# Optimization experiments

Measured on AMD Instinct MI355X. Metric: run time of the kernel, lower is better.

Reference implementation:

```python
import jax, jax.numpy as jnp
import numpy as np

N_NODES = 100000
N_EDGES = 1600000
IN_CH = 128
EDGE_CH = 32
HEADS = 4
OUT_CH = 32
NEG_SLOPE = 0.2
EPS = 1e-16  # matches torch_geometric softmax denominator epsilon


def setup_inputs() -> dict:
    key = jax.random.key(0)
    ks = jax.random.split(key, 8)
    x = jax.random.normal(ks[0], (N_NODES, IN_CH), dtype=jnp.float32)
    edge_attr = jax.random.normal(ks[1], (N_EDGES, EDGE_CH), dtype=jnp.float32)
    # glorot-ish scaled params
    Wl = jax.random.normal(ks[2], (HEADS * OUT_CH, IN_CH), dtype=jnp.float32) * (1.0 / np.sqrt(IN_CH))
    We = jax.random.normal(ks[3], (HEADS * OUT_CH, EDGE_CH), dtype=jnp.float32) * (1.0 / np.sqrt(EDGE_CH))
    att_l = jax.random.normal(ks[4], (1, HEADS, OUT_CH), dtype=jnp.float32) * 0.1
    att_r = jax.random.normal(ks[5], (1, HEADS, OUT_CH), dtype=jnp.float32) * 0.1
    att_e = jax.random.normal(ks[6], (1, HEADS, OUT_CH), dtype=jnp.float32) * 0.1
    bias = jnp.zeros((HEADS * OUT_CH,), dtype=jnp.float32)
    edge_index = jax.random.randint(ks[7], (2, N_EDGES), 0, N_NODES, dtype=jnp.int32)
    return {"x": x, "edge_attr": edge_attr, "Wl": Wl, "We": We,
            "att_l": att_l, "att_r": att_r, "att_e": att_e,
            "bias": bias, "edge_index": edge_index}


def reference(x, edge_attr, Wl, We, att_l, att_r, att_e, bias, edge_index):
    N = x.shape[0]
    H, C = att_l.shape[1], att_l.shape[2]
    # shared lin_l == lin_r projection  [N, H, C]
    xl = (x @ Wl.T).reshape(N, H, C)
    alpha_l = (xl * att_l).sum(-1)          # [N, H] source term
    alpha_r = (xl * att_r).sum(-1)          # [N, H] target term
    # edge feature projection            [E, H, C]
    e = (edge_attr @ We.T).reshape(-1, H, C)
    alpha_e = (e * att_e).sum(-1)           # [E, H]
    src, dst = edge_index[0], edge_index[1]
    # per-edge attention logits
    alpha = alpha_l[src] + alpha_r[dst] + alpha_e        # [E, H]
    alpha = jax.nn.leaky_relu(alpha, NEG_SLOPE)
    # segment softmax over incoming edges of each target node
    amax = jax.ops.segment_max(alpha, dst, num_segments=N)   # [N, H]
    ex = jnp.exp(alpha - amax[dst])
    denom = jax.ops.segment_sum(ex, dst, num_segments=N)     # [N, H]
    alpha_n = ex / (denom[dst] + EPS)                        # [E, H]
    # weighted scatter-add aggregation of source features
    msg = xl[src] * alpha_n[:, :, None]                      # [E, H, C]
    out = jax.ops.segment_sum(msg, dst, num_segments=N)      # [N, H, C]
    out = out.reshape(N, H * C) + bias                       # concat heads
    return out
```

## Files before the change

### kernel.cpp

```cpp
#include <hip/hip_runtime.h>
#include <hip/hip_fp16.h>

#define NN 100000
#define NE 1600000
#define NB 391
#define NEG 0.2f
#define NHALF 50000

#define OFF_XLB   ((size_t)0)
#define OFF_AL    ((size_t)6400000)
#define OFF_AR    ((size_t)6800000)
#define OFF_WE    ((size_t)7200000)
#define OFF_RECP  ((size_t)7200128)
#define OFF_RECS  ((size_t)10400128)
#define OFF_PAL   ((size_t)12000128)
#define OFF_TMP   OFF_RECP
#define OFF_BSUM  (OFF_RECP + 110000)
#define OFF_DEG   ((size_t)15200128)
#define OFF_ROW   ((size_t)15300128)

__device__ __forceinline__ unsigned short f2bf(float f) {
    unsigned u = __float_as_uint(f);
    u += 0x7fffu + ((u >> 16) & 1u);
    return (unsigned short)(u >> 16);
}
__device__ __forceinline__ float bf2f(unsigned short v) {
    return __uint_as_float((unsigned)v << 16);
}

__global__ void k_prep_zero(const float* __restrict__ We, const float* __restrict__ att_e,
                            float* __restrict__ we, int* __restrict__ deg) {
    int i = blockIdx.x * 256 + threadIdx.x;
    if (i < NN) deg[i] = 0;
    if (blockIdx.x == 0 && threadIdx.x < 128) {
        int t = threadIdx.x, h = t >> 5, k = t & 31;
        float s = 0.f;
        for (int c = 0; c < 32; ++c)
            s += att_e[h * 32 + c] * We[(size_t)(h * 32 + c) * 32 + k];
        we[t] = s;
    }
}

__global__ __launch_bounds__(256, 2) void k_node(
        const float* __restrict__ x, const float* __restrict__ Wl,
        const float* __restrict__ attl, const float* __restrict__ attr_,
        unsigned short* __restrict__ xlb, float* __restrict__ al, float* __restrict__ ar) {
    __shared__ float wT[128 * 128];
    __shared__ float xT[128 * 32];
    int t = threadIdx.x;
    int og = t & 31, ng = t >> 5;
    int nb = blockIdx.x * 32;

    {
        int o = t & 127, q = t >> 7;
        #pragma unroll
        for (int chunk = 0; chunk < 16; ++chunk) {
            int k0 = chunk * 8 + q * 4;
            float4 w = *(const float4*)&Wl[(size_t)o * 128 + k0];
            wT[(k0 + 0) * 128 + o] = w.x;
            wT[(k0 + 1) * 128 + o] = w.y;
            wT[(k0 + 2) * 128 + o] = w.z;
            wT[(k0 + 3) * 128 + o] = w.w;
        }
    }
    {
        int n = t & 31, q = t >> 5;
        #pragma unroll
        for (int chunk = 0; chunk < 4; ++chunk) {
            int k0 = chunk * 32 + q * 4;
            float4 v = *(const float4*)&x[(size_t)(nb + n) * 128 + k0];
            xT[(k0 + 0) * 32 + n] = v.x;
            xT[(k0 + 1) * 32 + n] = v.y;
            xT[(k0 + 2) * 32 + n] = v.z;
            xT[(k0 + 3) * 32 + n] = v.w;
        }
    }
    float4 attl4 = *(const float4*)&attl[og * 4];
    float4 attr4 = *(const float4*)&attr_[og * 4];
    __syncthreads();

    float4 a0 = make_float4(0,0,0,0), a1 = a0, a2 = a0, a3 = a0;
    #pragma unroll 8
    for (int k = 0; k < 128; ++k) {
        float4 w  = *(const float4*)&wT[k * 128 + og * 4];
        float4 xv = *(const float4*)&xT[k * 32  + ng * 4];
        a0.x += w.x * xv.x; a0.y += w.y * xv.x; a0.z += w.z * xv.x; a0.w += w.w * xv.x;
        a1.x += w.x * xv.y; a1.y += w.y * xv.y; a1.z += w.z * xv.y; a1.w += w.w * xv.y;
        a2.x += w.x * xv.z; a2.y += w.y * xv.z; a2.z += w.z * xv.z; a2.w += w.w * xv.z;
        a3.x += w.x * xv.w; a3.y += w.y * xv.w; a3.z += w.z * xv.w; a3.w += w.w * xv.w;
    }

    float4 accs[4] = {a0, a1, a2, a3};
    #pragma unroll
    for (int j = 0; j < 4; ++j) {
        int node = nb + ng * 4 + j;
        ushort4 pk;
        pk.x = f2bf(accs[j].x); pk.y = f2bf(accs[j].y);
        pk.z = f2bf(accs[j].z); pk.w = f2bf(accs[j].w);
        *(ushort4*)&xlb[(size_t)node * 128 + og * 4] = pk;
        float pl = accs[j].x * attl4.x + accs[j].y * attl4.y +
                   accs[j].z * attl4.z + accs[j].w * attl4.w;
        float pr = accs[j].x * attr4.x + accs[j].y * attr4.y +
                   accs[j].z * attr4.z + accs[j].w * attr4.w;
        #pragma unroll
        for (int off = 1; off <= 4; off <<= 1) {
            pl += __shfl_xor(pl, off);
            pr += __shfl_xor(pr, off);
        }
        if ((og & 7) == 0) {
            al[(size_t)node * 4 + (og >> 3)] = pl;
            ar[(size_t)node * 4 + (og >> 3)] = pr;
        }
    }
}

__global__ __launch_bounds__(256) void k_alpha(
        const float* __restrict__ eattr, const int* __restrict__ ei,
        const float* __restrict__ al, const float* __restrict__ ar,
        const float* __restrict__ we, int* __restrict__ deg,
        float2* __restrict__ palpha) {
    __shared__ __align__(16) float wsh[128];
    if (threadIdx.x < 128) wsh[threadIdx.x] = we[threadIdx.x];
    __syncthreads();
    int e = blockIdx.x * 256 + threadIdx.x;
    int src = ei[e], dst = ei[NE + e];
    const float4* ea = (const float4*)(eattr + (size_t)e * 32);
    float a[4] = {0.f, 0.f, 0.f, 0.f};
    #pragma unroll
    for (int r = 0; r < 8; ++r) {
        float4 v = ea[r];
        #pragma unroll
        for (int h = 0; h < 4; ++h) {
            float4 w = *(const float4*)&wsh[h * 32 + r * 4];
            a[h] += v.x * w.x + v.y * w.y + v.z * w.z + v.w * w.w;
        }
    }
    float4 ls = *(const float4*)&al[(size_t)src * 4];
    float4 rs = *(const float4*)&ar[(size_t)dst * 4];
    a[0] += ls.x + rs.x; a[1] += ls.y + rs.y;
    a[2] += ls.z + rs.z; a[3] += ls.w + rs.w;
    #pragma unroll
    for (int h = 0; h < 4; ++h) {
        float v = a[h] > 0.f ? a[h] : NEG * a[h];
        a[h] = __expf(fminf(v, 60.f));
    }
    __half2 h01 = __floats2half2_rn(a[0], a[1]);
    __half2 h23 = __floats2half2_rn(a[2], a[3]);
    float2 p;
    p.x = *reinterpret_cast<float*>(&h01);
    p.y = *reinterpret_cast<float*>(&h23);
    palpha[e] = p;
    atomicAdd(&deg[dst], 1);
}

__global__ void k_scan_block(const int* __restrict__ deg, int* __restrict__ row_tmp,
                             int* __restrict__ bsum) {
    __shared__ int sh[256];
    int t = threadIdx.x, i = blockIdx.x * 256 + t;
    int d = (i < NN) ? deg[i] : 0;
    int v = d;
    sh[t] = v; __syncthreads();
    for (int off = 1; off < 256; off <<= 1) {
        int add = (t >= off) ? sh[t - off] : 0;
        __syncthreads();
        v += add; sh[t] = v; __syncthreads();
    }
    if (i < NN) row_tmp[i] = v - d;
    if (t == 255) bsum[blockIdx.x] = v;
}

__global__ void k_scan_top(int* __restrict__ bsum) {
    __shared__ int sh[512];
    int t = threadIdx.x;
    int d = (t < NB) ? bsum[t] : 0;
    int v = d;
    sh[t] = v; __syncthreads();
    for (int off = 1; off < 512; off <<= 1) {
        int add = (t >= off) ? sh[t - off] : 0;
        __syncthreads();
        v += add; sh[t] = v; __syncthreads();
    }
    if (t < NB) bsum[t] = v - d;
}

__global__ void k_scan_add(const int* __restrict__ row_tmp, const int* __restrict__ bsum,
                           int* __restrict__ row, int* __restrict__ cursor) {
    int i = blockIdx.x * 256 + threadIdx.x;
    if (i < NN) {
        int v = row_tmp[i] + bsum[i >> 8];
        row[i] = v;
        cursor[i] = v;
    }
    if (i == 0) row[NN] = NE;
}

__global__ __launch_bounds__(256) void k_scat(
        const int* __restrict__ ei, const float2* __restrict__ palpha,
        int* __restrict__ cursor, int* __restrict__ rec_src,
        float2* __restrict__ rec_p, int lo, int hi) {
    int e = blockIdx.x * 256 + threadIdx.x;
    int dst = ei[NE + e];
    int src = ei[e];
    float2 p = palpha[e];
    if (dst >= lo && dst < hi) {
        int slot = atomicAdd(&cursor[dst], 1);
        rec_src[slot] = src;
        rec_p[slot] = p;
    }
}

__device__ __forceinline__ float pick_p(float2 q, int h) {
    __half2 h01 = *reinterpret_cast<const __half2*>(&q.x);
    __half2 h23 = *reinterpret_cast<const __half2*>(&q.y);
    float2 p01 = __half22float2(h01);
    float2 p23 = __half22float2(h23);
    float lo = (h & 2) ? p23.x : p01.x;
    float hi = (h & 2) ? p23.y : p01.y;
    return (h & 1) ? hi : lo;
}

__global__ __launch_bounds__(128) void k_out(
        const int* __restrict__ row, const int* __restrict__ rec_src,
        const float2* __restrict__ rec_p, const unsigned short* __restrict__ xlb,
        const float* __restrict__ bias, float* __restrict__ out) {
    int n = blockIdx.x;
    int t = threadIdx.x, h = t >> 5;
    int s0 = row[n], s1 = row[n + 1];

    float l0 = 0.f, l1 = 0.f, l2 = 0.f, l3 = 0.f;
    float O0 = 0.f, O1 = 0.f, O2 = 0.f, O3 = 0.f;
    int s = s0;
    for (; s + 4 <= s1; s += 4) {
        int src0 = rec_src[s + 0], src1 = rec_src[s + 1];
        int src2 = rec_src[s + 2], src3 = rec_src[s + 3];
        float2 q0 = rec_p[s + 0], q1 = rec_p[s + 1];
        float2 q2 = rec_p[s + 2], q3 = rec_p[s + 3];
        unsigned short v0 = xlb[(size_t)src0 * 128 + t];
        unsigned short v1 = xlb[(size_t)src1 * 128 + t];
        unsigned short v2 = xlb[(size_t)src2 * 128 + t];
        unsigned short v3 = xlb[(size_t)src3 * 128 + t];
        float p0 = pick_p(q0, h), p1 = pick_p(q1, h);
        float p2 = pick_p(q2, h), p3 = pick_p(q3, h);
        l0 += p0; l1 += p1; l2 += p2; l3 += p3;
        O0 += p0 * bf2f(v0); O1 += p1 * bf2f(v1);
        O2 += p2 * bf2f(v2); O3 += p3 * bf2f(v3);
    }
    for (; s < s1; ++s) {
        int srcn = rec_src[s];
        float p = pick_p(rec_p[s], h);
        l0 += p;
        O0 += p * bf2f(xlb[(size_t)srcn * 128 + t]);
    }
    float l = (l0 + l1) + (l2 + l3);
    float O = (O0 + O1) + (O2 + O3);
    out[(size_t)n * 128 + t] = O / (l + 1e-16f) + bias[t];
}

extern "C" void kernel_launch(void* const* d_in, const int* in_sizes, int n_in,
                              void* d_out, int out_size, void* d_ws, size_t ws_size,
                              hipStream_t stream) {
    const float* x     = (const float*)d_in[0];
    const float* eattr = (const float*)d_in[1];
    const float* Wl    = (const float*)d_in[2];
    const float* We    = (const float*)d_in[3];
    const float* att_l = (const float*)d_in[4];
    const float* att_r = (const float*)d_in[5];
    const float* att_e = (const float*)d_in[6];
    const float* bias  = (const float*)d_in[7];
    const int*   ei    = (const int*)d_in[8];
    float* out = (float*)d_out;

    float* ws = (float*)d_ws;
    unsigned short* xlb = (unsigned short*)(ws + OFF_XLB);
    float*  al      = ws + OFF_AL;
    float*  ar      = ws + OFF_AR;
    float*  we      = ws + OFF_WE;
    float2* rec_p   = (float2*)(ws + OFF_RECP);
    int*    rec_src = (int*)(ws + OFF_RECS);
    float2* palpha  = (float2*)(ws + OFF_PAL);
    int*    row_tmp = (int*)(ws + OFF_TMP);
    int*    bsum    = (int*)(ws + OFF_BSUM);
    int*    deg     = (int*)(ws + OFF_DEG);
    int*    rowp    = (int*)(ws + OFF_ROW);

    k_prep_zero<<<NB, 256, 0, stream>>>(We, att_e, we, deg);
    k_node<<<NN / 32, 256, 0, stream>>>(x, Wl, att_l, att_r, xlb, al, ar);
    k_alpha<<<NE / 256, 256, 0, stream>>>(eattr, ei, al, ar, we, deg, palpha);
    k_scan_block<<<NB, 256, 0, stream>>>(deg, row_tmp, bsum);
    k_scan_top<<<1, 512, 0, stream>>>(bsum);
    k_scan_add<<<NB, 256, 0, stream>>>(row_tmp, bsum, rowp, deg);
    k_scat<<<NE / 256, 256, 0, stream>>>(ei, palpha, deg, rec_src, rec_p, 0, NHALF);
    k_scat<<<NE / 256, 256, 0, stream>>>(ei, palpha, deg, rec_src, rec_p, NHALF, NN);
    k_out<<<NN, 128, 0, stream>>>(rowp, rec_src, rec_p, xlb, bias, out);
}
```

Measured before the change: 660.2 us.

## Record per-edge rank in histogram pass and fuse alpha compute with CSR scatter

```diff
diff --git a/kernel.cpp b/kernel.cpp
--- a/kernel.cpp
+++ b/kernel.cpp
@@ -5,7 +5,6 @@
 #define NE 1600000
 #define NB 391
 #define NEG 0.2f
-#define NHALF 50000
 
 #define OFF_XLB   ((size_t)0)
 #define OFF_AL    ((size_t)6400000)
@@ -13,11 +12,11 @@
 #define OFF_WE    ((size_t)7200000)
 #define OFF_RECP  ((size_t)7200128)
 #define OFF_RECS  ((size_t)10400128)
-#define OFF_PAL   ((size_t)12000128)
+#define OFF_RANK  ((size_t)12000128)
 #define OFF_TMP   OFF_RECP
 #define OFF_BSUM  (OFF_RECP + 110000)
-#define OFF_DEG   ((size_t)15200128)
-#define OFF_ROW   ((size_t)15300128)
+#define OFF_DEG   ((size_t)13600128)
+#define OFF_ROW   ((size_t)13700128)
 
 __device__ __forceinline__ unsigned short f2bf(float f) {
     unsigned u = __float_as_uint(f);
@@ -29,16 +28,22 @@
 }
 
 __global__ void k_prep_zero(const float* __restrict__ We, const float* __restrict__ att_e,
-                            float* __restrict__ we, int* __restrict__ deg) {
+                            float* __restrict__ weT, int* __restrict__ deg) {
     int i = blockIdx.x * 256 + threadIdx.x;
     if (i < NN) deg[i] = 0;
     if (blockIdx.x == 0 && threadIdx.x < 128) {
-        int t = threadIdx.x, h = t >> 5, k = t & 31;
+        int t = threadIdx.x, h = t & 3, k = t >> 2;
         float s = 0.f;
         for (int c = 0; c < 32; ++c)
             s += att_e[h * 32 + c] * We[(size_t)(h * 32 + c) * 32 + k];
-        we[t] = s;
-    }
+        weT[t] = s;
+    }
+}
+
+__global__ void k_hist(const int* __restrict__ ei, int* __restrict__ deg,
+                       int* __restrict__ rank) {
+    int e = blockIdx.x * 256 + threadIdx.x;
+    rank[e] = atomicAdd(&deg[ei[NE + e]], 1);
 }
 
 __global__ __launch_bounds__(256, 2) void k_node(
@@ -114,45 +119,6 @@
     }
 }
 
-__global__ __launch_bounds__(256) void k_alpha(
-        const float* __restrict__ eattr, const int* __restrict__ ei,
-        const float* __restrict__ al, const float* __restrict__ ar,
-        const float* __restrict__ we, int* __restrict__ deg,
-        float2* __restrict__ palpha) {
-    __shared__ __align__(16) float wsh[128];
-    if (threadIdx.x < 128) wsh[threadIdx.x] = we[threadIdx.x];
-    __syncthreads();
-    int e = blockIdx.x * 256 + threadIdx.x;
-    int src = ei[e], dst = ei[NE + e];
-    const float4* ea = (const float4*)(eattr + (size_t)e * 32);
-    float a[4] = {0.f, 0.f, 0.f, 0.f};
-    #pragma unroll
-    for (int r = 0; r < 8; ++r) {
-        float4 v = ea[r];
-        #pragma unroll
-        for (int h = 0; h < 4; ++h) {
-            float4 w = *(const float4*)&wsh[h * 32 + r * 4];
-            a[h] += v.x * w.x + v.y * w.y + v.z * w.z + v.w * w.w;
-        }
-    }
-    float4 ls = *(const float4*)&al[(size_t)src * 4];
-    float4 rs = *(const float4*)&ar[(size_t)dst * 4];
-    a[0] += ls.x + rs.x; a[1] += ls.y + rs.y;
-    a[2] += ls.z + rs.z; a[3] += ls.w + rs.w;
-    #pragma unroll
-    for (int h = 0; h < 4; ++h) {
-        float v = a[h] > 0.f ? a[h] : NEG * a[h];
-        a[h] = __expf(fminf(v, 60.f));
-    }
-    __half2 h01 = __floats2half2_rn(a[0], a[1]);
-    __half2 h23 = __floats2half2_rn(a[2], a[3]);
-    float2 p;
-    p.x = *reinterpret_cast<float*>(&h01);
-    p.y = *reinterpret_cast<float*>(&h23);
-    palpha[e] = p;
-    atomicAdd(&deg[dst], 1);
-}
-
 __global__ void k_scan_block(const int* __restrict__ deg, int* __restrict__ row_tmp,
                              int* __restrict__ bsum) {
     __shared__ int sh[256];
@@ -184,29 +150,57 @@
 }
 
 __global__ void k_scan_add(const int* __restrict__ row_tmp, const int* __restrict__ bsum,
-                           int* __restrict__ row, int* __restrict__ cursor) {
+                           int* __restrict__ row) {
     int i = blockIdx.x * 256 + threadIdx.x;
-    if (i < NN) {
-        int v = row_tmp[i] + bsum[i >> 8];
-        row[i] = v;
-        cursor[i] = v;
-    }
+    if (i < NN) row[i] = row_tmp[i] + bsum[i >> 8];
     if (i == 0) row[NN] = NE;
 }
 
-__global__ __launch_bounds__(256) void k_scat(
-        const int* __restrict__ ei, const float2* __restrict__ palpha,
-        int* __restrict__ cursor, int* __restrict__ rec_src,
-        float2* __restrict__ rec_p, int lo, int hi) {
-    int e = blockIdx.x * 256 + threadIdx.x;
-    int dst = ei[NE + e];
-    int src = ei[e];
-    float2 p = palpha[e];
-    if (dst >= lo && dst < hi) {
-        int slot = atomicAdd(&cursor[dst], 1);
-        rec_src[slot] = src;
-        rec_p[slot] = p;
-    }
+__global__ __launch_bounds__(256) void k_edge(
+        const float* __restrict__ eattr, const int* __restrict__ ei,
+        const int* __restrict__ rank, const int* __restrict__ row,
+        const float* __restrict__ al, const float* __restrict__ ar,
+        const float* __restrict__ weT,
+        int* __restrict__ rec_src, float2* __restrict__ rec_p) {
+    __shared__ float esh[256 * 33];
+    int t = threadIdx.x;
+    size_t base = (size_t)blockIdx.x * 256 * 32;
+    #pragma unroll
+    for (int j = 0; j < 8; ++j) {
+        int idx = j * 256 + t;
+        float4 v = *(const float4*)&eattr[base + (size_t)idx * 4];
+        float* d = &esh[(idx >> 3) * 33 + (idx & 7) * 4];
+        d[0] = v.x; d[1] = v.y; d[2] = v.z; d[3] = v.w;
+    }
+    int e = blockIdx.x * 256 + t;
+    int src = ei[e], dst = ei[NE + e];
+    int rk = rank[e];
+    __syncthreads();
+
+    const float* r = &esh[t * 33];
+    float a0 = 0.f, a1 = 0.f, a2 = 0.f, a3 = 0.f;
+    #pragma unroll
+    for (int k = 0; k < 32; ++k) {
+        float v = r[k];
+        float4 w = *(const float4*)&weT[k * 4];
+        a0 += v * w.x; a1 += v * w.y; a2 += v * w.z; a3 += v * w.w;
+    }
+    float4 ls = *(const float4*)&al[(size_t)src * 4];
+    float4 rs = *(const float4*)&ar[(size_t)dst * 4];
+    a0 += ls.x + rs.x; a1 += ls.y + rs.y;
+    a2 += ls.z + rs.z; a3 += ls.w + rs.w;
+    a0 = a0 > 0.f ? a0 : NEG * a0;  a1 = a1 > 0.f ? a1 : NEG * a1;
+    a2 = a2 > 0.f ? a2 : NEG * a2;  a3 = a3 > 0.f ? a3 : NEG * a3;
+    a0 = __expf(fminf(a0, 60.f)); a1 = __expf(fminf(a1, 60.f));
+    a2 = __expf(fminf(a2, 60.f)); a3 = __expf(fminf(a3, 60.f));
+    __half2 h01 = __floats2half2_rn(a0, a1);
+    __half2 h23 = __floats2half2_rn(a2, a3);
+    int slot = row[dst] + rk;
+    rec_src[slot] = src;
+    float2 p;
+    p.x = *reinterpret_cast<float*>(&h01);
+    p.y = *reinterpret_cast<float*>(&h23);
+    rec_p[slot] = p;
 }
 
 __device__ __forceinline__ float pick_p(float2 q, int h) {
@@ -274,22 +268,21 @@
     unsigned short* xlb = (unsigned short*)(ws + OFF_XLB);
     float*  al      = ws + OFF_AL;
     float*  ar      = ws + OFF_AR;
-    float*  we      = ws + OFF_WE;
+    float*  weT     = ws + OFF_WE;
     float2* rec_p   = (float2*)(ws + OFF_RECP);
     int*    rec_src = (int*)(ws + OFF_RECS);
-    float2* palpha  = (float2*)(ws + OFF_PAL);
+    int*    rank    = (int*)(ws + OFF_RANK);
     int*    row_tmp = (int*)(ws + OFF_TMP);
     int*    bsum    = (int*)(ws + OFF_BSUM);
     int*    deg     = (int*)(ws + OFF_DEG);
     int*    rowp    = (int*)(ws + OFF_ROW);
 
-    k_prep_zero<<<NB, 256, 0, stream>>>(We, att_e, we, deg);
+    k_prep_zero<<<NB, 256, 0, stream>>>(We, att_e, weT, deg);
+    k_hist<<<NE / 256, 256, 0, stream>>>(ei, deg, rank);
     k_node<<<NN / 32, 256, 0, stream>>>(x, Wl, att_l, att_r, xlb, al, ar);
-    k_alpha<<<NE / 256, 256, 0, stream>>>(eattr, ei, al, ar, we, deg, palpha);
     k_scan_block<<<NB, 256, 0, stream>>>(deg, row_tmp, bsum);
     k_scan_top<<<1, 512, 0, stream>>>(bsum);
-    k_scan_add<<<NB, 256, 0, stream>>>(row_tmp, bsum, rowp, deg);
-    k_scat<<<NE / 256, 256, 0, stream>>>(ei, palpha, deg, rec_src, rec_p, 0, NHALF);
-    k_scat<<<NE / 256, 256, 0, stream>>>(ei, palpha, deg, rec_src, rec_p, NHALF, NN);
+    k_scan_add<<<NB, 256, 0, stream>>>(row_tmp, bsum, rowp);
+    k_edge<<<NE / 256, 256, 0, stream>>>(eattr, ei, rank, rowp, al, ar, weT, rec_src, rec_p);
     k_out<<<NN, 128, 0, stream>>>(rowp, rec_src, rec_p, xlb, bias, out);
 }
```

Result: faster. 605.1 us (-8.3%).
